# Performance work log

Measured on AMD Instinct MI355X. Metric: run time of the kernel, lower is better.

Reference implementation:

```python
import jax, jax.numpy as jnp
import numpy as np

B, D, E = 65536, 1024, 16
H1, H2 = 128, 64          # expert hidden dims (hidden_dim=128, hidden_dim//2)
R1, R2 = 64, 32           # router hidden dims
EPS = 1e-5                # BatchNorm eps


def setup_inputs() -> dict:
    key = jax.random.key(0)
    ks = jax.random.split(key, 16)
    s = 0.02
    inp = {
        "x": jax.random.normal(ks[0], (B, D), jnp.float32),
        # router BatchNorm1d (eval mode: running stats)
        "r_gamma": jnp.ones((D,), jnp.float32),
        "r_beta": jnp.zeros((D,), jnp.float32),
        "r_mean": jnp.zeros((D,), jnp.float32),
        "r_var": jnp.ones((D,), jnp.float32),
        # router MLP D->64->32->16
        "rW1": jax.random.normal(ks[1], (D, R1), jnp.float32) * s,
        "rb1": jnp.full((R1,), 0.1, jnp.float32),
        "rW2": jax.random.normal(ks[2], (R1, R2), jnp.float32) * s,
        "rb2": jnp.full((R2,), 0.1, jnp.float32),
        "rW3": jax.random.normal(ks[3], (R2, E), jnp.float32) * s,
        "rb3": jnp.full((E,), 0.1, jnp.float32),
        # per-expert BatchNorm1d (eval mode)
        "e_gamma": jnp.ones((E, D), jnp.float32),
        "e_beta": jnp.zeros((E, D), jnp.float32),
        "e_mean": jnp.zeros((E, D), jnp.float32),
        "e_var": jnp.ones((E, D), jnp.float32),
        # per-expert MLP D->128->64->1, stacked along expert dim
        "eW1": jax.random.normal(ks[4], (E, D, H1), jnp.float32) * s,
        "eb1": jnp.full((E, H1), 0.1, jnp.float32),
        "eW2": jax.random.normal(ks[5], (E, H1, H2), jnp.float32) * s,
        "eb2": jnp.full((E, H2), 0.1, jnp.float32),
        "eW3": jax.random.normal(ks[6], (E, H2, 1), jnp.float32) * s,
        "eb3": jnp.full((E, 1), 0.1, jnp.float32),
    }
    return inp


def reference(x, r_gamma, r_beta, r_mean, r_var, rW1, rb1, rW2, rb2, rW3, rb3,
              e_gamma, e_beta, e_mean, e_var, eW1, eb1, eW2, eb2, eW3, eb3):
    # ---- router: BN (eval) -> Linear/ReLU -> Linear/ReLU -> Linear -> softmax
    xn = (x - r_mean) * (r_gamma / jnp.sqrt(r_var + EPS)) + r_beta   # [B,D]
    h = jax.nn.relu(xn @ rW1 + rb1)
    h = jax.nn.relu(h @ rW2 + rb2)
    routing_weights = jax.nn.softmax(h @ rW3 + rb3, axis=1)          # [B,E]

    # ---- experts: fold per-expert BN into first linear to avoid [E,B,D] copy
    scale = e_gamma / jnp.sqrt(e_var + EPS)                          # [E,D]
    shift = e_beta - e_mean * scale                                  # [E,D]
    W1_eff = eW1 * scale[:, :, None]                                 # [E,D,H1]
    b1_eff = eb1 + jnp.einsum('ed,edh->eh', shift, eW1)              # [E,H1]

    h1 = jax.nn.relu(jnp.einsum('bd,edh->ebh', x, W1_eff) + b1_eff[:, None, :])  # [E,B,H1]
    h2 = jax.nn.relu(jnp.einsum('ebh,ehk->ebk', h1, eW2) + eb2[:, None, :])      # [E,B,H2]
    logits = jnp.einsum('ebk,eko->ebo', h2, eW3) + eb3[:, None, :]               # [E,B,1]
    expert_outputs = jax.nn.sigmoid(logits[:, :, 0]).T               # [B,E]

    weighted_pred = jnp.sum(routing_weights * expert_outputs, axis=1)  # [B]
    return weighted_pred, routing_weights, expert_outputs
```

## Files before the change

### kernel.cpp

```cpp
#include <hip/hip_runtime.h>


typedef unsigned short u16;
typedef __attribute__((ext_vector_type(8))) short bf16x8;
typedef __attribute__((ext_vector_type(4))) float f32x4;
typedef __attribute__((ext_vector_type(8))) unsigned short u16x8;
typedef __attribute__((ext_vector_type(4))) unsigned short u16x4;

#define MFMA16(a, b, c) __builtin_amdgcn_mfma_f32_16x16x32_bf16(a, b, c, 0, 0, 0)

#define B_ROWS 65536
#define NE 16
#define EPS 1e-5f

#define SBAR() __builtin_amdgcn_s_barrier()
#define VMCNT(n)                                             \
    do {                                                     \
        asm volatile("s_waitcnt vmcnt(" #n ")" ::: "memory");\
        __builtin_amdgcn_sched_barrier(0);                   \
    } while (0)

__device__ inline u16 f2bf(float f) {
    union { float f; unsigned u; } c; c.f = f;
    unsigned u = c.u;
    return (u16)((u + 0x7fffu + ((u >> 16) & 1u)) >> 16);
}

__device__ inline void gload16(const u16* g, u16* s) {
    __builtin_amdgcn_global_load_lds(
        (const __attribute__((address_space(1))) unsigned int*)g,
        (__attribute__((address_space(3))) unsigned int*)s,
        16, 0, 0);
}


__device__ void body_prep_x(int blk, int tid, const float* __restrict__ x,
                            u16* __restrict__ xbf) {
#pragma unroll
    for (int i = 0; i < 8; ++i) {
        size_t fi = (((size_t)blk * 2048) + i * 256 + tid) * 8;
        float4 f0 = *(const float4*)(x + fi);
        float4 f1 = *(const float4*)(x + fi + 4);
        u16x8 u;
        u[0] = f2bf(f0.x); u[1] = f2bf(f0.y); u[2] = f2bf(f0.z); u[3] = f2bf(f0.w);
        u[4] = f2bf(f1.x); u[5] = f2bf(f1.y); u[6] = f2bf(f1.z); u[7] = f2bf(f1.w);
        *(u16x8*)&xbf[fi] = u;
    }
}

__device__ void body_prep_w1s(int t, const float* __restrict__ eW1, const float* __restrict__ eg,
                              const float* __restrict__ ev, u16* __restrict__ w1sr) {
    int ko = t & 127, h = t >> 7;
    int nt = h >> 8, sub = h & 255;
    int e = nt * 2 + (sub >> 7), hl = sub & 127;
    u16x8 u;
#pragma unroll
    for (int j = 0; j < 8; ++j) {
        int d = ko * 8 + j;
        float sc = eg[e * 1024 + d] * rsqrtf(ev[e * 1024 + d] + EPS);
        u[j] = f2bf(eW1[((size_t)e * 1024 + d) * 128 + hl] * sc);
    }
    *(u16x8*)&w1sr[((size_t)h << 10) + ko * 8] = u;
}

__device__ void body_prep_b1(int g, int lane, const float* __restrict__ eW1,
                             const float* __restrict__ eg, const float* __restrict__ eb,
                             const float* __restrict__ em, const float* __restrict__ ev,
                             const float* __restrict__ eb1, float* __restrict__ b1e) {
    int e = g >> 7, h = g & 127;
    float s = 0.f;
    for (int d = lane; d < 1024; d += 64) {
        float sc = eg[e * 1024 + d] * rsqrtf(ev[e * 1024 + d] + EPS);
        float sh = eb[e * 1024 + d] - em[e * 1024 + d] * sc;
        s += sh * eW1[((size_t)e * 1024 + d) * 128 + h];
    }
#pragma unroll
    for (int m = 1; m < 64; m <<= 1) s += __shfl_xor(s, m, 64);
    if (lane == 0) b1e[e * 128 + h] = eb1[e * 128 + h] + s;
}

__device__ void body_prep_rw1s(int t, const float* __restrict__ rW1, const float* __restrict__ rg,
                               const float* __restrict__ rv, u16* __restrict__ rw1sr) {
    int ko = t & 127, j = t >> 7;
    u16x8 u;
#pragma unroll
    for (int k = 0; k < 8; ++k) {
        int d = ko * 8 + k;
        float sc = rg[d] * rsqrtf(rv[d] + EPS);
        u[k] = f2bf(rW1[d * 64 + j] * sc);
    }
    *(u16x8*)&rw1sr[(j << 10) + ko * 8] = u;
}

__device__ void body_prep_rb1(int j, int lane, const float* __restrict__ rW1,
                              const float* __restrict__ rg, const float* __restrict__ rbta,
                              const float* __restrict__ rm, const float* __restrict__ rv,
                              const float* __restrict__ rb1, float* __restrict__ rb1e) {
    float s = 0.f;
    for (int d = lane; d < 1024; d += 64) {
        float sc = rg[d] * rsqrtf(rv[d] + EPS);
        float sh = rbta[d] - rm[d] * sc;
        s += sh * rW1[d * 64 + j];
    }
#pragma unroll
    for (int m = 1; m < 64; m <<= 1) s += __shfl_xor(s, m, 64);
    if (lane == 0) rb1e[j] = rb1[j] + s;
}

__device__ void body_prep_w2s(int t, const float* __restrict__ eW2, u16* __restrict__ w2s) {
    int p = t & 15, j = (t >> 4) & 63, e = t >> 10;
    int lb = p ^ (j & 7);
    int h0 = lb * 8;
    u16x8 u;
#pragma unroll
    for (int jj = 0; jj < 8; ++jj)
        u[jj] = f2bf(eW2[((size_t)e * 128 + h0 + jj) * 64 + j]);
    *(u16x8*)&w2s[((e * 64 + j) << 7) + p * 8] = u;
}

__global__ __launch_bounds__(256) void prep_all(
    const float* __restrict__ x, u16* __restrict__ xbf,
    const float* __restrict__ eW1, const float* __restrict__ eg,
    const float* __restrict__ eb, const float* __restrict__ em,
    const float* __restrict__ ev, const float* __restrict__ eb1,
    u16* __restrict__ w1sr, float* __restrict__ b1e,
    const float* __restrict__ rW1, const float* __restrict__ rg,
    const float* __restrict__ rbta, const float* __restrict__ rm,
    const float* __restrict__ rv, const float* __restrict__ rb1,
    u16* __restrict__ rw1sr, float* __restrict__ rb1e,
    const float* __restrict__ eW2, u16* __restrict__ w2s) {
    int bid = blockIdx.x, tid = threadIdx.x;
    if (bid < 4096) {
        body_prep_x(bid, tid, x, xbf);
    } else if (bid < 5120) {
        body_prep_w1s((bid - 4096) * 256 + tid, eW1, eg, ev, w1sr);
    } else if (bid < 5632) {
        body_prep_b1((bid - 5120) * 4 + (tid >> 6), tid & 63, eW1, eg, eb, em, ev, eb1, b1e);
    } else if (bid < 5664) {
        body_prep_rw1s((bid - 5632) * 256 + tid, rW1, rg, rv, rw1sr);
    } else if (bid < 5680) {
        body_prep_rb1((bid - 5664) * 4 + (tid >> 6), tid & 63, rW1, rg, rbta, rm, rv, rb1, rb1e);
    } else {
        body_prep_w2s((bid - 5680) * 256 + tid, eW2, w2s);
    }
}

__global__ __launch_bounds__(512, 2) void fused_main(
    const u16* __restrict__ xbf, const u16* __restrict__ w1sr,
    const float* __restrict__ b1e, const u16* __restrict__ w2s,
    const float* __restrict__ eb2, const float* __restrict__ eW3,
    const float* __restrict__ eb3, float* __restrict__ out_eo,
    const u16* __restrict__ rw1sr, const float* __restrict__ rb1e,
    const float* __restrict__ rW2, const float* __restrict__ rb2,
    const float* __restrict__ rW3, const float* __restrict__ rb3,
    float* __restrict__ out_rw) {
    __shared__ __align__(16) char smem[131072];

    int tid = threadIdx.x;
    int wave = tid >> 6, lane = tid & 63, quad = lane >> 4, l15 = lane & 15;
    int lr = lane >> 2, lc = lane & 3;
    int swz = (lr >> 1) & 3;
    int sch = (lc ^ swz) * 8;
    int phq = (quad ^ ((l15 >> 1) & 3)) * 8;

    if (blockIdx.x >= 256) {
        int i = blockIdx.x - 256;
        int rb = (i & 7) * 32 + (i >> 6);
        int nt = (i >> 3) & 7;
        int wm = wave >> 2, wn = wave & 3;

        u16* ring = (u16*)smem;
        const u16* gA0 = w1sr + ((size_t)(nt * 256 + wave * 32 + lr) << 10) + sch;
        const u16* gB0 = xbf + ((size_t)(rb * 256 + wave * 32 + lr) << 10) + sch;
        int laneA = (wm * 128 + l15) * 32 + phq;
        int laneB = (wn * 64 + l15) * 32 + phq;

        f32x4 acc[8][4] = {};
        bf16x8 fa0[8], fb0[4], fa1[8], fb1[4];

        auto STAGE = [&](int t) {
            u16* ls = ring + (t & 3) * 16384 + wave * 1024;
            const u16* ga = gA0 + t * 32;
            const u16* gb = gB0 + t * 32;
            gload16(ga, ls);
            gload16(ga + 16384, ls + 512);
            gload16(gb, ls + 8192);
            gload16(gb + 16384, ls + 8192 + 512);
        };
        auto LOADFRAG = [&](bf16x8 (&fa)[8], bf16x8 (&fb)[4], int t) {
            const u16* lA = ring + (t & 3) * 16384;
#pragma unroll
            for (int ii = 0; ii < 8; ++ii)
                fa[ii] = *(const bf16x8*)&lA[laneA + ii * 512];
#pragma unroll
            for (int jj = 0; jj < 4; ++jj)
                fb[jj] = *(const bf16x8*)&lA[8192 + laneB + jj * 512];
        };
        auto MFMACL = [&](bf16x8 (&fa)[8], bf16x8 (&fb)[4]) {
            __builtin_amdgcn_s_setprio(1);
#pragma unroll
            for (int ii = 0; ii < 8; ++ii)
#pragma unroll
                for (int jj = 0; jj < 4; ++jj)
                    acc[ii][jj] = MFMA16(fa[ii], fb[jj], acc[ii][jj]);
            __builtin_amdgcn_s_setprio(0);
        };

#define BODY(S, CA, CB, NA, NB)                    \
    do {                                           \
        SBAR();                                    \
        STAGE((S) + 3);                            \
        VMCNT(8);                                  \
        SBAR();                                    \
        __builtin_amdgcn_sched_barrier(0);         \
        LOADFRAG(NA, NB, (S) + 1);                 \
        __builtin_amdgcn_sched_barrier(0);         \
        MFMACL(CA, CB);                            \
    } while (0)

        STAGE(0); STAGE(1); STAGE(2);
        VMCNT(8);
        SBAR();
        __builtin_amdgcn_sched_barrier(0);
        LOADFRAG(fa0, fb0, 0);

#pragma clang loop unroll(disable)
        for (int s2 = 0; s2 < 28; s2 += 2) {
            BODY(s2, fa0, fb0, fa1, fb1);
            BODY(s2 + 1, fa1, fb1, fa0, fb0);
        }
        BODY(28, fa0, fb0, fa1, fb1);
        VMCNT(4);
        SBAR();
        __builtin_amdgcn_sched_barrier(0);
        LOADFRAG(fa0, fb0, 30);
        __builtin_amdgcn_sched_barrier(0);
        MFMACL(fa1, fb1);
        VMCNT(0);
        SBAR();
        __builtin_amdgcn_sched_barrier(0);
        LOADFRAG(fa1, fb1, 31);
        __builtin_amdgcn_sched_barrier(0);
        MFMACL(fa0, fb0);
        MFMACL(fa1, fb1);
#undef BODY

        int e = nt * 2 + wm;
        u16* h1 = ring;
        SBAR();
#pragma unroll
        for (int ii = 0; ii < 8; ++ii) {
            float4 bv = *(const float4*)&b1e[e * 128 + ii * 16 + quad * 4];
            float bva[4] = {bv.x, bv.y, bv.z, bv.w};
            int h0 = wm * 128 + ii * 16 + quad * 4;
            int oc = h0 >> 3, hin = h0 & 7;
#pragma unroll
            for (int jj = 0; jj < 4; ++jj) {
                int m = wn * 64 + jj * 16 + l15;
                u16x4 pk;
#pragma unroll
                for (int r = 0; r < 4; ++r)
                    pk[r] = f2bf(fmaxf(acc[ii][jj][r] + bva[r], 0.f));
                int poc = (oc & 24) | ((oc ^ m) & 7);
                *(u16x4*)&h1[m * 256 + poc * 8 + hin] = pk;
            }
        }
        bf16x8 w2f[4][4];
        const u16* gW2 = w2s + e * 8192;
#pragma unroll
        for (int ks = 0; ks < 4; ++ks)
#pragma unroll
            for (int tj = 0; tj < 4; ++tj) {
                int jc = tj * 16 + l15;
                int pq = (ks * 4 + quad) ^ (jc & 7);
                w2f[ks][tj] = *(const bf16x8*)&gW2[jc * 128 + pq * 8];
            }
        asm volatile("s_waitcnt lgkmcnt(0)" ::: "memory");
        __builtin_amdgcn_sched_barrier(0);
        SBAR();

        f32x4 acc2[4][4] = {};
#pragma unroll
        for (int ks = 0; ks < 4; ++ks) {
            bf16x8 a2[4];
#pragma unroll
            for (int mi = 0; mi < 4; ++mi) {
                int m = wn * 64 + mi * 16 + l15;
                int oc2 = wm * 16 + ks * 4 + quad;
                int poc2 = (oc2 & 24) | ((oc2 ^ m) & 7);
                a2[mi] = *(const bf16x8*)&h1[m * 256 + poc2 * 8];
            }
#pragma unroll
            for (int mi = 0; mi < 4; ++mi)
#pragma unroll
                for (int tj = 0; tj < 4; ++tj)
                    acc2[mi][tj] = MFMA16(a2[mi], w2f[ks][tj], acc2[mi][tj]);
        }

        float b2v[4], w3v[4];
#pragma unroll
        for (int tj = 0; tj < 4; ++tj) {
            int jc = tj * 16 + l15;
            b2v[tj] = eb2[e * 64 + jc];
            w3v[tj] = eW3[e * 64 + jc];
        }
        float be3 = eb3[e];
#pragma unroll
        for (int mi = 0; mi < 4; ++mi) {
            float sv[4] = {0.f, 0.f, 0.f, 0.f};
#pragma unroll
            for (int tj = 0; tj < 4; ++tj)
#pragma unroll
                for (int r = 0; r < 4; ++r)
                    sv[r] += fmaxf(acc2[mi][tj][r] + b2v[tj], 0.f) * w3v[tj];
#pragma unroll
            for (int mask = 1; mask < 16; mask <<= 1)
#pragma unroll
                for (int r = 0; r < 4; ++r) sv[r] += __shfl_xor(sv[r], mask, 64);
            if (l15 == 0) {
#pragma unroll
                for (int r = 0; r < 4; ++r) {
                    int m = wn * 64 + mi * 16 + quad * 4 + r;
                    float z = sv[r] + be3;
                    out_eo[(size_t)(rb * 256 + m) * 16 + e] = 1.f / (1.f + __expf(-z));
                }
            }
        }
    } else {
        int rb = blockIdx.x;
        u16* ldsX = (u16*)smem;
        u16* ldsW = (u16*)smem + 16384;
        float* h_r = (float*)smem;
        float* h2s = (float*)(smem + 69632);
        const u16* gX0 = xbf + ((size_t)(rb * 256 + wave * 32 + lr) << 10) + sch;
        int stw = wave >> 2, q3 = wave & 3;
        const u16* gW0 = rw1sr + ((size_t)(q3 * 16 + lr) << 10) + sch;

        f32x4 accr[4][2] = {};
        for (int kt = 0; kt < 16; ++kt) {
            int s0 = kt * 2;
            u16* lx = ldsX + wave * 1024;
            gload16(gX0 + s0 * 32, lx);
            gload16(gX0 + 16384 + s0 * 32, lx + 512);
            gload16(gX0 + (s0 + 1) * 32, lx + 8192);
            gload16(gX0 + 16384 + (s0 + 1) * 32, lx + 8192 + 512);
            gload16(gW0 + (s0 + stw) * 32, ldsW + stw * 2048 + q3 * 512);
            __syncthreads();
#pragma unroll
            for (int st = 0; st < 2; ++st) {
                bf16x8 aw[4], bx[2];
#pragma unroll
                for (int jf = 0; jf < 4; ++jf)
                    aw[jf] = *(const bf16x8*)&ldsW[st * 2048 + (jf * 16 + l15) * 32 + phq];
#pragma unroll
                for (int mf = 0; mf < 2; ++mf)
                    bx[mf] = *(const bf16x8*)&ldsX[st * 8192 + (wave * 32 + mf * 16 + l15) * 32 + phq];
#pragma unroll
                for (int jf = 0; jf < 4; ++jf)
#pragma unroll
                    for (int mf = 0; mf < 2; ++mf)
                        accr[jf][mf] = MFMA16(aw[jf], bx[mf], accr[jf][mf]);
            }
            __syncthreads();
        }

#pragma unroll
        for (int jf = 0; jf < 4; ++jf) {
            int j0 = jf * 16 + quad * 4;
            float4 bv = *(const float4*)&rb1e[j0];
#pragma unroll
            for (int mf = 0; mf < 2; ++mf) {
                int m = wave * 32 + mf * 16 + l15;
                float4 hv;
                hv.x = fmaxf(accr[jf][mf][0] + bv.x, 0.f);
                hv.y = fmaxf(accr[jf][mf][1] + bv.y, 0.f);
                hv.z = fmaxf(accr[jf][mf][2] + bv.z, 0.f);
                hv.w = fmaxf(accr[jf][mf][3] + bv.w, 0.f);
                *(float4*)&h_r[m * 68 + j0] = hv;
            }
        }
        __syncthreads();

        {
            int m = tid & 255, qg = tid >> 8;
            float h2r[16];
#pragma unroll
            for (int k = 0; k < 16; ++k) h2r[k] = 0.f;
            for (int i2 = 0; i2 < 64; ++i2) {
                float hv = h_r[m * 68 + i2];
                const float4* wrow = (const float4*)&rW2[i2 * 32 + qg * 16];
                float w[16];
                *(float4*)&w[0] = wrow[0];
                *(float4*)&w[4] = wrow[1];
                *(float4*)&w[8] = wrow[2];
                *(float4*)&w[12] = wrow[3];
#pragma unroll
                for (int k = 0; k < 16; ++k) h2r[k] += hv * w[k];
            }
#pragma unroll
            for (int k = 0; k < 16; ++k)
                h2r[k] = fmaxf(h2r[k] + rb2[qg * 16 + k], 0.f);
#pragma unroll
            for (int k = 0; k < 16; k += 4)
                *(float4*)&h2s[m * 36 + qg * 16 + k] = *(float4*)&h2r[k];
        }
        __syncthreads();

        if (tid < 256) {
            int mm = tid;
            float lg[16];
#pragma unroll
            for (int o = 0; o < 16; ++o) lg[o] = 0.f;
            for (int q = 0; q < 32; ++q) {
                float hv = h2s[mm * 36 + q];
                const float4* wr = (const float4*)&rW3[q * 16];
                float w[16];
                *(float4*)&w[0] = wr[0];
                *(float4*)&w[4] = wr[1];
                *(float4*)&w[8] = wr[2];
                *(float4*)&w[12] = wr[3];
#pragma unroll
                for (int o = 0; o < 16; ++o) lg[o] += hv * w[o];
            }
#pragma unroll
            for (int o = 0; o < 16; ++o) lg[o] += rb3[o];
            float mx = lg[0];
#pragma unroll
            for (int o = 1; o < 16; ++o) mx = fmaxf(mx, lg[o]);
            float ss = 0.f;
#pragma unroll
            for (int o = 0; o < 16; ++o) { lg[o] = __expf(lg[o] - mx); ss += lg[o]; }
            float inv = 1.f / ss;
            size_t base = (size_t)(rb * 256 + mm) * 16;
#pragma unroll
            for (int o = 0; o < 16; o += 4) {
                float4 v;
                v.x = lg[o] * inv; v.y = lg[o + 1] * inv;
                v.z = lg[o + 2] * inv; v.w = lg[o + 3] * inv;
                *(float4*)&out_rw[base + o] = v;
            }
        }
    }
}

__global__ void combine_kernel(const float* __restrict__ rw, const float* __restrict__ eo,
                               float* __restrict__ wp) {
    int b = blockIdx.x * 256 + threadIdx.x;
    const float4* r4 = (const float4*)(rw + (size_t)b * 16);
    const float4* o4 = (const float4*)(eo + (size_t)b * 16);
    float s = 0.f;
#pragma unroll
    for (int k = 0; k < 4; ++k) {
        float4 r = r4[k], o = o4[k];
        s += r.x * o.x + r.y * o.y + r.z * o.z + r.w * o.w;
    }
    wp[b] = s;
}


extern "C" void kernel_launch(void* const* d_in, const int* in_sizes, int n_in,
                              void* d_out, int out_size, void* d_ws, size_t ws_size,
                              hipStream_t stream) {
    const float* x       = (const float*)d_in[0];
    const float* r_gamma = (const float*)d_in[1];
    const float* r_beta  = (const float*)d_in[2];
    const float* r_mean  = (const float*)d_in[3];
    const float* r_var   = (const float*)d_in[4];
    const float* rW1     = (const float*)d_in[5];
    const float* rb1     = (const float*)d_in[6];
    const float* rW2     = (const float*)d_in[7];
    const float* rb2     = (const float*)d_in[8];
    const float* rW3     = (const float*)d_in[9];
    const float* rb3     = (const float*)d_in[10];
    const float* e_gamma = (const float*)d_in[11];
    const float* e_beta  = (const float*)d_in[12];
    const float* e_mean  = (const float*)d_in[13];
    const float* e_var   = (const float*)d_in[14];
    const float* eW1     = (const float*)d_in[15];
    const float* eb1     = (const float*)d_in[16];
    const float* eW2     = (const float*)d_in[17];
    const float* eb2     = (const float*)d_in[18];
    const float* eW3     = (const float*)d_in[19];
    const float* eb3     = (const float*)d_in[20];

    char* ws = (char*)d_ws;
    u16* xbf    = (u16*)ws;
    u16* w1sr   = (u16*)(ws + 134217728);
    u16* rw1sr  = (u16*)(ws + 138412032);
    u16* w2s    = (u16*)(ws + 138543104);
    float* b1e  = (float*)(ws + 138805248);
    float* rb1e = (float*)(ws + 138813440);

    float* out_wp = (float*)d_out;
    float* out_rw = out_wp + B_ROWS;
    float* out_eo = out_rw + (size_t)B_ROWS * NE;

    prep_all<<<5744, 256, 0, stream>>>(
        x, xbf,
        eW1, e_gamma, e_beta, e_mean, e_var, eb1, w1sr, b1e,
        rW1, r_gamma, r_beta, r_mean, r_var, rb1, rw1sr, rb1e,
        eW2, w2s);

    fused_main<<<2304, 512, 0, stream>>>(
        xbf, w1sr, b1e, w2s, eb2, eW3, eb3, out_eo,
        rw1sr, rb1e, rW2, rb2, rW3, rb3, out_rw);

    combine_kernel<<<256, 256, 0, stream>>>(out_rw, out_eo, out_wp);
}
```

Measured before the change: 752.5 us.

## Split GEMM main loop into two half-phases with split A/B staging

Measured after the change: 736.2 us. 1.02x faster.

```diff
diff --git a/kernel.cpp b/kernel.cpp
--- a/kernel.cpp
+++ b/kernel.cpp
@@ -17,6 +17,11 @@
 #define VMCNT(n)                                             \
     do {                                                     \
         asm volatile("s_waitcnt vmcnt(" #n ")" ::: "memory");\
+        __builtin_amdgcn_sched_barrier(0);                   \
+    } while (0)
+#define LGKM0()                                              \
+    do {                                                     \
+        asm volatile("s_waitcnt lgkmcnt(0)" ::: "memory");   \
         __builtin_amdgcn_sched_barrier(0);                   \
     } while (0)
 
@@ -176,74 +181,85 @@
         int laneB = (wn * 64 + l15) * 32 + phq;
 
         f32x4 acc[8][4] = {};
-        bf16x8 fa0[8], fb0[4], fa1[8], fb1[4];
-
-        auto STAGE = [&](int t) {
+        bf16x8 fa[4], fa2[4], fb[4];
+
+        auto STAGE_A = [&](int t) {
             u16* ls = ring + (t & 3) * 16384 + wave * 1024;
             const u16* ga = gA0 + t * 32;
-            const u16* gb = gB0 + t * 32;
             gload16(ga, ls);
             gload16(ga + 16384, ls + 512);
-            gload16(gb, ls + 8192);
-            gload16(gb + 16384, ls + 8192 + 512);
         };
-        auto LOADFRAG = [&](bf16x8 (&fa)[8], bf16x8 (&fb)[4], int t) {
-            const u16* lA = ring + (t & 3) * 16384;
-#pragma unroll
-            for (int ii = 0; ii < 8; ++ii)
+        auto STAGE_B = [&](int t) {
+            u16* ls = ring + (t & 3) * 16384 + 8192 + wave * 1024;
+            const u16* gb = gB0 + t * 32;
+            gload16(gb, ls);
+            gload16(gb + 16384, ls + 512);
+        };
+        auto LOAD_A03_B = [&](int s) {
+            const u16* lA = ring + (s & 3) * 16384;
+#pragma unroll
+            for (int ii = 0; ii < 4; ++ii)
                 fa[ii] = *(const bf16x8*)&lA[laneA + ii * 512];
 #pragma unroll
             for (int jj = 0; jj < 4; ++jj)
                 fb[jj] = *(const bf16x8*)&lA[8192 + laneB + jj * 512];
         };
-        auto MFMACL = [&](bf16x8 (&fa)[8], bf16x8 (&fb)[4]) {
+        auto LOAD_A47 = [&](int s) {
+            const u16* lA = ring + (s & 3) * 16384;
+#pragma unroll
+            for (int ii = 0; ii < 4; ++ii)
+                fa2[ii] = *(const bf16x8*)&lA[laneA + (ii + 4) * 512];
+        };
+        auto MFMA_LO = [&] {
             __builtin_amdgcn_s_setprio(1);
 #pragma unroll
-            for (int ii = 0; ii < 8; ++ii)
+            for (int ii = 0; ii < 4; ++ii)
 #pragma unroll
                 for (int jj = 0; jj < 4; ++jj)
                     acc[ii][jj] = MFMA16(fa[ii], fb[jj], acc[ii][jj]);
             __builtin_amdgcn_s_setprio(0);
         };
-
-#define BODY(S, CA, CB, NA, NB)                    \
+        auto MFMA_HI = [&] {
+            __builtin_amdgcn_s_setprio(1);
+#pragma unroll
+            for (int ii = 0; ii < 4; ++ii)
+#pragma unroll
+                for (int jj = 0; jj < 4; ++jj)
+                    acc[ii + 4][jj] = MFMA16(fa2[ii], fb[jj], acc[ii + 4][jj]);
+            __builtin_amdgcn_s_setprio(0);
+        };
+
+#define STEP(S, DO_STAGE, VM)                      \
     do {                                           \
+        LOAD_A03_B(S);                             \
+        if (DO_STAGE) STAGE_A((S) + 3);            \
         SBAR();                                    \
-        STAGE((S) + 3);                            \
-        VMCNT(8);                                  \
+        LGKM0();                                   \
+        MFMA_LO();                                 \
         SBAR();                                    \
-        __builtin_amdgcn_sched_barrier(0);         \
-        LOADFRAG(NA, NB, (S) + 1);                 \
-        __builtin_amdgcn_sched_barrier(0);         \
-        MFMACL(CA, CB);                            \
+        LOAD_A47(S);                               \
+        if (DO_STAGE) STAGE_B((S) + 3);            \
+        VM;                                        \
+        SBAR();                                    \
+        LGKM0();                                   \
+        MFMA_HI();                                 \
+        SBAR();                                    \
     } while (0)
 
-        STAGE(0); STAGE(1); STAGE(2);
+        STAGE_A(0); STAGE_B(0);
+        STAGE_A(1); STAGE_B(1);
+        STAGE_A(2); STAGE_B(2);
         VMCNT(8);
         SBAR();
-        __builtin_amdgcn_sched_barrier(0);
-        LOADFRAG(fa0, fb0, 0);
 
 #pragma clang loop unroll(disable)
-        for (int s2 = 0; s2 < 28; s2 += 2) {
-            BODY(s2, fa0, fb0, fa1, fb1);
-            BODY(s2 + 1, fa1, fb1, fa0, fb0);
-        }
-        BODY(28, fa0, fb0, fa1, fb1);
-        VMCNT(4);
-        SBAR();
-        __builtin_amdgcn_sched_barrier(0);
-        LOADFRAG(fa0, fb0, 30);
-        __builtin_amdgcn_sched_barrier(0);
-        MFMACL(fa1, fb1);
-        VMCNT(0);
-        SBAR();
-        __builtin_amdgcn_sched_barrier(0);
-        LOADFRAG(fa1, fb1, 31);
-        __builtin_amdgcn_sched_barrier(0);
-        MFMACL(fa0, fb0);
-        MFMACL(fa1, fb1);
-#undef BODY
+        for (int s = 0; s < 29; ++s) {
+            STEP(s, true, VMCNT(8));
+        }
+        STEP(29, false, VMCNT(4));
+        STEP(30, false, VMCNT(0));
+        STEP(31, false, (void)0);
+#undef STEP
 
         int e = nt * 2 + wm;
         u16* h1 = ring;
```
